# Kernel optimization log

Measured on AMD Instinct MI355X. Metric: run time of the kernel, lower is better.

## Reference

```python
import jax, jax.numpy as jnp
import numpy as np

EPS = 1e-8
N_ITER = 3
S = 8      # n_slots
D = 64     # slot_size
HID = 128  # mlp hidden


def _ln(x, w, b):
    m = jnp.mean(x, axis=-1, keepdims=True)
    v = jnp.var(x, axis=-1, keepdims=True)
    return (x - m) * jax.lax.rsqrt(v + 1e-5) * w + b


def setup_inputs() -> dict:
    key = jax.random.key(0)
    ks = jax.random.split(key, 20)
    B, N, Din = 128, 4096, 64
    g = lambda k, sh, s: (jax.random.normal(k, sh, jnp.float32) * s)
    return {
        "inputs": jax.random.normal(ks[0], (B, N, Din), jnp.float32),
        "eps_noise": jax.random.normal(ks[1], (B, S, D), jnp.float32),
        "slot_mu": g(ks[2], (1, 1, D), 0.1),
        "slot_logvar": g(ks[3], (1, 1, D), 0.1),
        "k_w": g(ks[4], (D, Din), 1.0 / np.sqrt(Din)),
        "v_w": g(ks[5], (D, Din), 1.0 / np.sqrt(Din)),
        "q_w": g(ks[6], (D, D), 1.0 / np.sqrt(D)),
        "ni_w": jnp.ones((Din,), jnp.float32), "ni_b": jnp.zeros((Din,), jnp.float32),
        "ns_w": jnp.ones((D,), jnp.float32),  "ns_b": jnp.zeros((D,), jnp.float32),
        "nr_w": jnp.ones((D,), jnp.float32),  "nr_b": jnp.zeros((D,), jnp.float32),
        "gru_wih": g(ks[7], (3 * D, D), 1.0 / np.sqrt(D)),
        "gru_whh": g(ks[8], (3 * D, D), 1.0 / np.sqrt(D)),
        "gru_bih": jnp.zeros((3 * D,), jnp.float32),
        "gru_bhh": jnp.zeros((3 * D,), jnp.float32),
        "mlp_w1": g(ks[9], (HID, D), 1.0 / np.sqrt(D)),
        "mlp_w2": g(ks[10], (D, HID), 1.0 / np.sqrt(HID)),
        "mlp_b2": jnp.zeros((D,), jnp.float32),
    }


def _gru(x, h, wih, whh, bih, bhh):
    gi = x @ wih.T + bih  # [BS, 3D]
    gh = h @ whh.T + bhh
    i_r, i_z, i_n = jnp.split(gi, 3, axis=-1)
    h_r, h_z, h_n = jnp.split(gh, 3, axis=-1)
    r = jax.nn.sigmoid(i_r + h_r)
    z = jax.nn.sigmoid(i_z + h_z)
    n = jnp.tanh(i_n + r * h_n)
    return (1.0 - z) * n + z * h


def _step(slots, k, v, q_w, ns_w, ns_b, nr_w, nr_b,
          gru_wih, gru_whh, gru_bih, gru_bhh, mlp_w1, mlp_w2, mlp_b2):
    B = slots.shape[0]
    q = _ln(slots, ns_w, ns_b) @ q_w.T                     # [B,S,D]
    logits = jnp.einsum('bnd,bsd->bns', k, q)              # [B,N,S]
    w = jax.nn.softmax(logits, axis=-1) + EPS              # softmax over slots
    w = w / jnp.sum(w, axis=-2, keepdims=True)             # renorm over tokens
    atten_maps = jnp.einsum('bns,bnd->bsd', w, v)          # [B,S,D]
    h = _gru(atten_maps.reshape(B * S, D), slots.reshape(B * S, D),
             gru_wih, gru_whh, gru_bih, gru_bhh)
    h = h + (jax.nn.relu(_ln(h, nr_w, nr_b) @ mlp_w1.T) @ mlp_w2.T + mlp_b2)
    return h.reshape(B, S, D), w


def reference(inputs, eps_noise, slot_mu, slot_logvar, k_w, v_w, q_w,
              ni_w, ni_b, ns_w, ns_b, nr_w, nr_b,
              gru_wih, gru_whh, gru_bih, gru_bhh, mlp_w1, mlp_w2, mlp_b2):
    std = jnp.exp(0.5 * slot_logvar)
    slots = slot_mu + std * eps_noise                      # [B,S,D]
    x = _ln(inputs, ni_w, ni_b)
    k = (x @ k_w.T) / np.sqrt(D).astype(np.float32)        # [B,N,D]
    v = x @ v_w.T
    args = (q_w, ns_w, ns_b, nr_w, nr_b, gru_wih, gru_whh,
            gru_bih, gru_bhh, mlp_w1, mlp_w2, mlp_b2)
    for _ in range(N_ITER):
        slots, w = _step(slots, k, v, *args)
    slots, w = _step(jax.lax.stop_gradient(slots), k, v, *args)
    return slots, w
```

## Files before the change

### kernel.cpp

```cpp
#include <hip/hip_runtime.h>
#include <hip/hip_bf16.h>

#define BB 128
#define NN 4096
#define DD 64
#define SS 8
#define HH 128

typedef __attribute__((ext_vector_type(8))) short short8;
typedef __attribute__((ext_vector_type(4))) float f32x4;

__device__ __forceinline__ float warp_red_sum(float v) {
    #pragma unroll
    for (int off = 32; off; off >>= 1) v += __shfl_xor(v, off);
    return v;
}

__device__ __forceinline__ float bcastlane(float v, int l) {
    return __int_as_float(__builtin_amdgcn_readlane(__float_as_int(v), l));
}

__device__ __forceinline__ unsigned short bfu(float f) {
    __hip_bfloat16 h = __float2bfloat16(f);
    return *(unsigned short*)&h;
}

__device__ __forceinline__ unsigned pk2(float a, float b) {
    return (unsigned)bfu(a) | ((unsigned)bfu(b) << 16);
}

__global__ __launch_bounds__(256) void prep_kernel(
    const float* __restrict__ v_w, const float* __restrict__ q_w,
    const float* __restrict__ wih, const float* __restrict__ whh,
    const float* __restrict__ w1, const float* __restrict__ w2,
    float* __restrict__ vwT, float* __restrict__ qwT,
    float* __restrict__ wihT, float* __restrict__ whhT,
    float* __restrict__ w1T, float* __restrict__ w2T)
{
    int i0 = blockIdx.x * blockDim.x + threadIdx.x;
    int nthr = gridDim.x * blockDim.x;
    for (int t = i0; t < 4096; t += nthr) {
        int i = t >> 6, o = t & 63;
        vwT[t] = v_w[o * 64 + i];
        qwT[t] = q_w[o * 64 + i];
    }
    for (int t = i0; t < 12288; t += nthr) {
        int r = t / 192, c = t % 192;
        wihT[t] = wih[c * 64 + r];
        whhT[t] = whh[c * 64 + r];
    }
    for (int t = i0; t < 8192; t += nthr) {
        int r = t >> 7, c = t & 127;
        w1T[t] = w1[c * 64 + r];
    }
    for (int t = i0; t < 8192; t += nthr) {
        int r = t >> 6, c = t & 63;
        w2T[t] = w2[c * 128 + r];
    }
}

__global__ __launch_bounds__(256) void init_q_kernel(
    const float* __restrict__ eps, const float* __restrict__ mu,
    const float* __restrict__ lv, const float* __restrict__ qwT,
    const float* __restrict__ k_w,
    const float* __restrict__ nsw, const float* __restrict__ nsb,
    float* __restrict__ slots, unsigned short* __restrict__ qb,
    float* __restrict__ zbuf)
{
    const int tid = threadIdx.x, lane = tid & 63;
    const int row = blockIdx.x * 4 + (tid >> 6);
    const int idx = row * 64 + lane;
    float s0 = mu[lane] + __expf(0.5f * lv[lane]) * eps[idx];
    slots[idx] = s0;
    float m = warp_red_sum(s0) * (1.0f / 64.0f);
    float dx = s0 - m;
    float var = warp_red_sum(dx * dx) * (1.0f / 64.0f);
    float xln = dx * rsqrtf(var + 1e-5f) * nsw[lane] + nsb[lane];
    float q = 0.f;
    #pragma unroll 8
    for (int i = 0; i < 64; ++i) q = fmaf(bcastlane(xln, i), qwT[i * 64 + lane], q);
    float qp = 0.f;
    #pragma unroll 8
    for (int o = 0; o < 64; ++o) qp = fmaf(bcastlane(q, o), k_w[o * 64 + lane], qp);
    qb[idx] = bfu(qp * 0.125f);
    int g = blockIdx.x * 256 + tid;
    for (int j = g; j < 66560; j += 65536) zbuf[j] = 0.f;
}

__global__ __launch_bounds__(256) void phase_a_ln(
    const float* __restrict__ inp, const float* __restrict__ niw, const float* __restrict__ nib,
    unsigned short* __restrict__ xb, unsigned short* __restrict__ xbt)
{
    __shared__ unsigned short xt[64 * 136];
    const int tid = threadIdx.x, lane = tid & 63, widx = tid >> 6;
    const int tg = lane >> 4, dq = lane & 15;
    const float4 wni = *(const float4*)&niw[dq * 4];
    const float4 bni = *(const float4*)&nib[dq * 4];
    const int tok0 = blockIdx.x * 128;
    #pragma unroll
    for (int it = 0; it < 8; ++it) {
        const int m = widx * 32 + it * 4 + tg;
        float4 x = *(const float4*)&inp[(size_t)(tok0 + m) * 64 + dq * 4];
        float s1 = x.x + x.y + x.z + x.w;
        float s2 = fmaf(x.x, x.x, fmaf(x.y, x.y, fmaf(x.z, x.z, x.w * x.w)));
        #pragma unroll
        for (int o = 1; o < 16; o <<= 1) { s1 += __shfl_xor(s1, o); s2 += __shfl_xor(s2, o); }
        float mean = s1 * (1.0f / 64.0f);
        float var = s2 * (1.0f / 64.0f) - mean * mean;
        float rstd = rsqrtf(var + 1e-5f);
        float y0 = (x.x - mean) * rstd * wni.x + bni.x;
        float y1 = (x.y - mean) * rstd * wni.y + bni.y;
        float y2 = (x.z - mean) * rstd * wni.z + bni.z;
        float y3 = (x.w - mean) * rstd * wni.w + bni.w;
        uint2 p; p.x = pk2(y0, y1); p.y = pk2(y2, y3);
        *(uint2*)&xb[(size_t)(tok0 + m) * 64 + dq * 4] = p;
        xt[(dq * 4 + 0) * 136 + m] = bfu(y0);
        xt[(dq * 4 + 1) * 136 + m] = bfu(y1);
        xt[(dq * 4 + 2) * 136 + m] = bfu(y2);
        xt[(dq * 4 + 3) * 136 + m] = bfu(y3);
    }
    __syncthreads();
    const int b = blockIdx.x >> 5, tin = (blockIdx.x & 31) * 128;
    const int d = tid >> 2, q4 = tid & 3;
    #pragma unroll
    for (int c = 0; c < 4; ++c) {
        uint4 o = *(uint4*)&xt[d * 136 + q4 * 32 + c * 8];
        *(uint4*)&xbt[((size_t)b * 64 + d) * 4096 + tin + q4 * 32 + c * 8] = o;
    }
}

__global__ __launch_bounds__(256) void attn_mfma(
    const __hip_bfloat16* __restrict__ xb, const unsigned short* __restrict__ xbt,
    const unsigned short* __restrict__ qb,
    float* __restrict__ numer, float* __restrict__ denom, float* __restrict__ wout)
{
    __shared__ unsigned short smem[24192];
    unsigned short* Qs = smem;
    const int tid = threadIdx.x, lane = tid & 63, widx = tid >> 6;
    unsigned short* wls = smem + 1152 + widx * 1152;
    unsigned short* vt  = smem + 5760 + widx * 4608;
    const int b = blockIdx.y;

    for (int t = tid; t < 1024; t += 256) {
        int s = t >> 6, dd = t & 63;
        Qs[s * 72 + dd] = (s < 8) ? qb[b * 512 + t] : (unsigned short)0;
    }
    for (int t = lane; t < 576; t += 64) wls[576 + t] = 0;
    __syncthreads();

    const int quad = lane >> 4, l16 = lane & 15;
    short8 bq0 = *(const short8*)&Qs[l16 * 72 + quad * 8];
    short8 bq1 = *(const short8*)&Qs[l16 * 72 + 32 + quad * 8];

    f32x4 accv[4];
    #pragma unroll
    for (int nt = 0; nt < 4; ++nt) accv[nt] = (f32x4){0.f, 0.f, 0.f, 0.f};
    float dsum = 0.f;

    const int twave0 = blockIdx.x * 512 + widx * 128;
    const int vd = lane >> 3, vc = (lane & 7) * 8;
    #pragma unroll
    for (int iter = 0; iter < 2; ++iter) {
        const int t0 = twave0 + iter * 64;
        uint4 vld[8];
        #pragma unroll
        for (int i = 0; i < 8; ++i)
            vld[i] = *(const uint4*)&xbt[((size_t)b * 64 + i * 8 + vd) * 4096 + t0 + vc];

        #pragma unroll
        for (int t4 = 0; t4 < 4; ++t4) {
            const size_t krow = ((size_t)b * NN + t0 + t4 * 16 + l16) * 64;
            short8 ak0 = *(const short8*)&xb[krow + quad * 8];
            short8 ak1 = *(const short8*)&xb[krow + 32 + quad * 8];
            f32x4 lg = (f32x4){0.f, 0.f, 0.f, 0.f};
            lg = __builtin_amdgcn_mfma_f32_16x16x32_bf16(ak0, bq0, lg, 0, 0, 0);
            lg = __builtin_amdgcn_mfma_f32_16x16x32_bf16(ak1, bq1, lg, 0, 0, 0);
            float wv[4];
            #pragma unroll
            for (int r = 0; r < 4; ++r) {
                float e = __expf(lg[r]);
                float s = e;
                s += __shfl_xor(s, 1); s += __shfl_xor(s, 2); s += __shfl_xor(s, 4);
                wv[r] = e / s + 1e-8f;
                dsum += wv[r];
            }
            if (l16 < 8) {
                *(unsigned*)&wls[l16 * 72 + t4 * 16 + quad * 4]     = pk2(wv[0], wv[1]);
                *(unsigned*)&wls[l16 * 72 + t4 * 16 + quad * 4 + 2] = pk2(wv[2], wv[3]);
                if (wout) {
                    float* wp = wout + ((size_t)b * NN + t0 + t4 * 16 + quad * 4) * 8 + l16;
                    wp[0] = wv[0]; wp[8] = wv[1]; wp[16] = wv[2]; wp[24] = wv[3];
                }
            }
        }
        #pragma unroll
        for (int i = 0; i < 8; ++i)
            *(uint4*)&vt[(i * 8 + vd) * 72 + vc] = vld[i];
        #pragma unroll
        for (int ks = 0; ks < 2; ++ks) {
            short8 aw = *(const short8*)&wls[l16 * 72 + ks * 32 + quad * 8];
            #pragma unroll
            for (int nt = 0; nt < 4; ++nt) {
                short8 bv = *(const short8*)&vt[(nt * 16 + l16) * 72 + ks * 32 + quad * 8];
                accv[nt] = __builtin_amdgcn_mfma_f32_16x16x32_bf16(aw, bv, accv[nt], 0, 0, 0);
            }
        }
    }
    dsum += __shfl_xor(dsum, 16);
    dsum += __shfl_xor(dsum, 32);
    __syncthreads();
    float* red = (float*)(smem + 5760);
    float* dred = red + 2048;
    if (quad < 2) {
        #pragma unroll
        for (int nt = 0; nt < 4; ++nt)
            #pragma unroll
            for (int r = 0; r < 4; ++r)
                red[widx * 512 + (quad * 4 + r) * 64 + nt * 16 + l16] = accv[nt][r];
    }
    if (quad == 0 && l16 < 8) dred[widx * 8 + l16] = dsum;
    __syncthreads();
    for (int e = tid; e < 512; e += 256)
        atomicAdd(numer + (size_t)b * 512 + e, red[e] + red[512 + e] + red[1024 + e] + red[1536 + e]);
    if (tid < 8)
        atomicAdd(denom + b * 8 + tid, dred[tid] + dred[8 + tid] + dred[16 + tid] + dred[24 + tid]);
}

__global__ __launch_bounds__(256) void gru_q_kernel(
    const float* __restrict__ numerX, const float* __restrict__ denom,
    const float* __restrict__ slotsIn,
    const float* __restrict__ vwT, const float* __restrict__ wihT, const float* __restrict__ whhT,
    const float* __restrict__ w1T, const float* __restrict__ w2T,
    const float* __restrict__ bih, const float* __restrict__ bhh,
    const float* __restrict__ nrw, const float* __restrict__ nrb,
    const float* __restrict__ b2,
    const float* __restrict__ qwT, const float* __restrict__ k_w,
    const float* __restrict__ nsw, const float* __restrict__ nsb,
    float* __restrict__ slotsOut, unsigned short* __restrict__ qb,
    float* __restrict__ zbuf)
{
    const int tid = threadIdx.x, lane = tid & 63;
    const int row = blockIdx.x * 4 + (tid >> 6);
    float nx = numerX[row * 64 + lane];
    float xp = 0.f;
    #pragma unroll 8
    for (int i = 0; i < 64; ++i) xp = fmaf(bcastlane(nx, i), vwT[i * 64 + lane], xp);
    float x = xp / denom[row];
    float h = slotsIn[row * 64 + lane];
    float air = 0, aiz = 0, ain = 0, ahr = 0, ahz = 0, ahn = 0;
    #pragma unroll 8
    for (int i = 0; i < 64; ++i) {
        float xi = bcastlane(x, i), hi = bcastlane(h, i);
        const float* wi = wihT + i * 192;
        const float* wh = whhT + i * 192;
        air = fmaf(xi, wi[lane], air);
        aiz = fmaf(xi, wi[64 + lane], aiz);
        ain = fmaf(xi, wi[128 + lane], ain);
        ahr = fmaf(hi, wh[lane], ahr);
        ahz = fmaf(hi, wh[64 + lane], ahz);
        ahn = fmaf(hi, wh[128 + lane], ahn);
    }
    air += bih[lane]; aiz += bih[64 + lane]; ain += bih[128 + lane];
    ahr += bhh[lane]; ahz += bhh[64 + lane]; ahn += bhh[128 + lane];
    float r = 1.f / (1.f + __expf(-(air + ahr)));
    float z = 1.f / (1.f + __expf(-(aiz + ahz)));
    float n = tanhf(ain + r * ahn);
    float hn = (1.f - z) * n + z * h;
    float m = warp_red_sum(hn) * (1.0f / 64.0f);
    float dx = hn - m;
    float var = warp_red_sum(dx * dx) * (1.0f / 64.0f);
    float u = dx * rsqrtf(var + 1e-5f) * nrw[lane] + nrb[lane];
    float o0 = 0.f, o1 = 0.f;
    #pragma unroll 8
    for (int i = 0; i < 64; ++i) {
        float ui = bcastlane(u, i);
        const float* w1r = w1T + i * 128;
        o0 = fmaf(ui, w1r[lane], o0);
        o1 = fmaf(ui, w1r[64 + lane], o1);
    }
    o0 = fmaxf(o0, 0.f); o1 = fmaxf(o1, 0.f);
    float y = 0.f;
    #pragma unroll 8
    for (int j = 0; j < 64; ++j) y = fmaf(bcastlane(o0, j), w2T[j * 64 + lane], y);
    #pragma unroll 8
    for (int j = 0; j < 64; ++j) y = fmaf(bcastlane(o1, j), w2T[(64 + j) * 64 + lane], y);
    y += b2[lane];
    float out = hn + y;
    slotsOut[row * 64 + lane] = out;
    float m2 = warp_red_sum(out) * (1.0f / 64.0f);
    float dx2 = out - m2;
    float var2 = warp_red_sum(dx2 * dx2) * (1.0f / 64.0f);
    float u2 = dx2 * rsqrtf(var2 + 1e-5f) * nsw[lane] + nsb[lane];
    float q = 0.f;
    #pragma unroll 8
    for (int i = 0; i < 64; ++i) q = fmaf(bcastlane(u2, i), qwT[i * 64 + lane], q);
    float qp = 0.f;
    #pragma unroll 8
    for (int o = 0; o < 64; ++o) qp = fmaf(bcastlane(q, o), k_w[o * 64 + lane], qp);
    qb[row * 64 + lane] = bfu(qp * 0.125f);
    int g = blockIdx.x * 256 + tid;
    for (int j = g; j < 66560; j += 65536) zbuf[j] = 0.f;
}

__global__ __launch_bounds__(256) void renorm_kernel(float* __restrict__ wout,
                                                     const float* __restrict__ denom)
{
    const size_t i4 = (size_t)blockIdx.x * blockDim.x + threadIdx.x;
    const size_t b = i4 >> 13;
    const int half = (int)(i4 & 1);
    float4 v = reinterpret_cast<float4*>(wout)[i4];
    const float4 dv = reinterpret_cast<const float4*>(denom)[b * 2 + half];
    v.x /= dv.x; v.y /= dv.y; v.z /= dv.z; v.w /= dv.w;
    reinterpret_cast<float4*>(wout)[i4] = v;
}

extern "C" void kernel_launch(void* const* d_in, const int* in_sizes, int n_in,
                              void* d_out, int out_size, void* d_ws, size_t ws_size,
                              hipStream_t stream)
{
    const float* inputs  = (const float*)d_in[0];
    const float* eps_n   = (const float*)d_in[1];
    const float* mu      = (const float*)d_in[2];
    const float* lv      = (const float*)d_in[3];
    const float* k_w     = (const float*)d_in[4];
    const float* v_w     = (const float*)d_in[5];
    const float* q_w     = (const float*)d_in[6];
    const float* ni_w    = (const float*)d_in[7];
    const float* ni_b    = (const float*)d_in[8];
    const float* ns_w    = (const float*)d_in[9];
    const float* ns_b    = (const float*)d_in[10];
    const float* nr_w    = (const float*)d_in[11];
    const float* nr_b    = (const float*)d_in[12];
    const float* gru_wih = (const float*)d_in[13];
    const float* gru_whh = (const float*)d_in[14];
    const float* gru_bih = (const float*)d_in[15];
    const float* gru_bhh = (const float*)d_in[16];
    const float* mlp_w1  = (const float*)d_in[17];
    const float* mlp_w2  = (const float*)d_in[18];
    const float* mlp_b2  = (const float*)d_in[19];

    char* wsb = (char*)d_ws;
    unsigned short* xb  = (unsigned short*)wsb;
    unsigned short* xbt = (unsigned short*)(wsb + 67108864);
    float* f      = (float*)(wsb + 134217728);
    float* slotsA = f;
    float* slotsB = f + 65536;
    unsigned short* qb = (unsigned short*)(f + 131072);
    float* numer0 = f + 163840;
    float* denom0 = f + 229376;
    float* numer1 = f + 230400;
    float* denom1 = f + 295936;
    float* vwT    = f + 296960;
    float* qwT    = f + 301056;
    float* wihT   = f + 305152;
    float* whhT   = f + 317440;
    float* w1T    = f + 329728;
    float* w2T    = f + 337920;

    float* out_slots = (float*)d_out;
    float* out_w     = out_slots + 65536;

    prep_kernel<<<64, 256, 0, stream>>>(v_w, q_w, gru_wih, gru_whh, mlp_w1, mlp_w2,
                                        vwT, qwT, wihT, whhT, w1T, w2T);
    init_q_kernel<<<256, 256, 0, stream>>>(eps_n, mu, lv, qwT, k_w, ns_w, ns_b,
                                           slotsA, qb, numer0);
    phase_a_ln<<<4096, 256, 0, stream>>>(inputs, ni_w, ni_b, xb, xbt);

    float* cur = slotsA;
    float* numers[2] = {numer0, numer1};
    float* denoms[2] = {denom0, denom1};
    for (int step = 0; step < 4; ++step) {
        int pb = step & 1;
        attn_mfma<<<dim3(8, 128), 256, 0, stream>>>((const __hip_bfloat16*)xb, xbt, qb,
                                                    numers[pb], denoms[pb],
                                                    step == 3 ? out_w : nullptr);
        float* nxt = (step == 3) ? out_slots : ((step & 1) ? slotsA : slotsB);
        gru_q_kernel<<<256, 256, 0, stream>>>(numers[pb], denoms[pb], cur,
                                              vwT, wihT, whhT, w1T, w2T,
                                              gru_bih, gru_bhh, nr_w, nr_b, mlp_b2,
                                              qwT, k_w, ns_w, ns_b,
                                              nxt, qb, numers[1 - pb]);
        cur = nxt;
    }
    renorm_kernel<<<4096, 256, 0, stream>>>(out_w, denom1);
}
```

Baseline: 456.1 us.

## Swap MFMA operands so slots map to rows, and swizzle LN transpose LDS

The logits MFMA now takes Q as the A operand and K as B, so each lane holds four slot values for one token. The softmax over slots then needs one cross-lane shuffle instead of three per element, uses a reciprocal instead of a divide, and writes the weight output as a float4 per token. The LayerNorm transpose buffer gets an XOR swizzle to cut LDS bank conflicts on the scattered column writes. Denominator sums are reduced per slot across 16 lanes at the end, and the wls store pattern changes to scattered 16-bit writes.

```diff
diff --git a/kernel.cpp b/kernel.cpp
--- a/kernel.cpp
+++ b/kernel.cpp
@@ -97,6 +97,7 @@
     const float4 wni = *(const float4*)&niw[dq * 4];
     const float4 bni = *(const float4*)&nib[dq * 4];
     const int tok0 = blockIdx.x * 128;
+    const int sw = dq & 7;
     #pragma unroll
     for (int it = 0; it < 8; ++it) {
         const int m = widx * 32 + it * 4 + tg;
@@ -114,18 +115,21 @@
         float y3 = (x.w - mean) * rstd * wni.w + bni.w;
         uint2 p; p.x = pk2(y0, y1); p.y = pk2(y2, y3);
         *(uint2*)&xb[(size_t)(tok0 + m) * 64 + dq * 4] = p;
-        xt[(dq * 4 + 0) * 136 + m] = bfu(y0);
-        xt[(dq * 4 + 1) * 136 + m] = bfu(y1);
-        xt[(dq * 4 + 2) * 136 + m] = bfu(y2);
-        xt[(dq * 4 + 3) * 136 + m] = bfu(y3);
+        const int col = ((((m >> 3) ^ sw) << 3) | (m & 7));
+        xt[(dq * 4 + 0) * 136 + col] = bfu(y0);
+        xt[(dq * 4 + 1) * 136 + col] = bfu(y1);
+        xt[(dq * 4 + 2) * 136 + col] = bfu(y2);
+        xt[(dq * 4 + 3) * 136 + col] = bfu(y3);
     }
     __syncthreads();
     const int b = blockIdx.x >> 5, tin = (blockIdx.x & 31) * 128;
     const int d = tid >> 2, q4 = tid & 3;
+    const int sr = (d >> 2) & 7;
     #pragma unroll
     for (int c = 0; c < 4; ++c) {
-        uint4 o = *(uint4*)&xt[d * 136 + q4 * 32 + c * 8];
-        *(uint4*)&xbt[((size_t)b * 64 + d) * 4096 + tin + q4 * 32 + c * 8] = o;
+        const int cc = q4 * 4 + c;
+        uint4 o = *(uint4*)&xt[d * 136 + ((cc ^ sr) << 3)];
+        *(uint4*)&xbt[((size_t)b * 64 + d) * 4096 + tin + cc * 8] = o;
     }
 }
 
@@ -149,13 +153,13 @@
     __syncthreads();
 
     const int quad = lane >> 4, l16 = lane & 15;
-    short8 bq0 = *(const short8*)&Qs[l16 * 72 + quad * 8];
-    short8 bq1 = *(const short8*)&Qs[l16 * 72 + 32 + quad * 8];
+    short8 aq0 = *(const short8*)&Qs[l16 * 72 + quad * 8];
+    short8 aq1 = *(const short8*)&Qs[l16 * 72 + 32 + quad * 8];
 
     f32x4 accv[4];
     #pragma unroll
     for (int nt = 0; nt < 4; ++nt) accv[nt] = (f32x4){0.f, 0.f, 0.f, 0.f};
-    float dsum = 0.f;
+    float dacc[4] = {0.f, 0.f, 0.f, 0.f};
 
     const int twave0 = blockIdx.x * 512 + widx * 128;
     const int vd = lane >> 3, vc = (lane & 7) * 8;
@@ -169,28 +173,29 @@
 
         #pragma unroll
         for (int t4 = 0; t4 < 4; ++t4) {
-            const size_t krow = ((size_t)b * NN + t0 + t4 * 16 + l16) * 64;
-            short8 ak0 = *(const short8*)&xb[krow + quad * 8];
-            short8 ak1 = *(const short8*)&xb[krow + 32 + quad * 8];
+            const int tok = t0 + t4 * 16 + l16;
+            const size_t xrow = ((size_t)b * NN + tok) * 64;
+            short8 bk0 = *(const short8*)&xb[xrow + quad * 8];
+            short8 bk1 = *(const short8*)&xb[xrow + 32 + quad * 8];
             f32x4 lg = (f32x4){0.f, 0.f, 0.f, 0.f};
-            lg = __builtin_amdgcn_mfma_f32_16x16x32_bf16(ak0, bq0, lg, 0, 0, 0);
-            lg = __builtin_amdgcn_mfma_f32_16x16x32_bf16(ak1, bq1, lg, 0, 0, 0);
+            lg = __builtin_amdgcn_mfma_f32_16x16x32_bf16(aq0, bk0, lg, 0, 0, 0);
+            lg = __builtin_amdgcn_mfma_f32_16x16x32_bf16(aq1, bk1, lg, 0, 0, 0);
+            float e[4];
+            #pragma unroll
+            for (int r = 0; r < 4; ++r) e[r] = __expf(lg[r]);
+            float s4 = (e[0] + e[1]) + (e[2] + e[3]);
+            float stot = s4 + __shfl_xor(s4, 16);
+            float rs = __builtin_amdgcn_rcpf(stot);
             float wv[4];
             #pragma unroll
-            for (int r = 0; r < 4; ++r) {
-                float e = __expf(lg[r]);
-                float s = e;
-                s += __shfl_xor(s, 1); s += __shfl_xor(s, 2); s += __shfl_xor(s, 4);
-                wv[r] = e / s + 1e-8f;
-                dsum += wv[r];
-            }
-            if (l16 < 8) {
-                *(unsigned*)&wls[l16 * 72 + t4 * 16 + quad * 4]     = pk2(wv[0], wv[1]);
-                *(unsigned*)&wls[l16 * 72 + t4 * 16 + quad * 4 + 2] = pk2(wv[2], wv[3]);
-                if (wout) {
-                    float* wp = wout + ((size_t)b * NN + t0 + t4 * 16 + quad * 4) * 8 + l16;
-                    wp[0] = wv[0]; wp[8] = wv[1]; wp[16] = wv[2]; wp[24] = wv[3];
-                }
+            for (int r = 0; r < 4; ++r) { wv[r] = fmaf(e[r], rs, 1e-8f); dacc[r] += wv[r]; }
+            if (quad < 2) {
+                #pragma unroll
+                for (int r = 0; r < 4; ++r)
+                    wls[(quad * 4 + r) * 72 + t4 * 16 + l16] = bfu(wv[r]);
+                if (wout)
+                    *(float4*)&wout[((size_t)b * NN + tok) * 8 + quad * 4] =
+                        make_float4(wv[0], wv[1], wv[2], wv[3]);
             }
         }
         #pragma unroll
@@ -206,8 +211,13 @@
             }
         }
     }
-    dsum += __shfl_xor(dsum, 16);
-    dsum += __shfl_xor(dsum, 32);
+    #pragma unroll
+    for (int r = 0; r < 4; ++r) {
+        dacc[r] += __shfl_xor(dacc[r], 1);
+        dacc[r] += __shfl_xor(dacc[r], 2);
+        dacc[r] += __shfl_xor(dacc[r], 4);
+        dacc[r] += __shfl_xor(dacc[r], 8);
+    }
     __syncthreads();
     float* red = (float*)(smem + 5760);
     float* dred = red + 2048;
@@ -217,8 +227,11 @@
             #pragma unroll
             for (int r = 0; r < 4; ++r)
                 red[widx * 512 + (quad * 4 + r) * 64 + nt * 16 + l16] = accv[nt][r];
-    }
-    if (quad == 0 && l16 < 8) dred[widx * 8 + l16] = dsum;
+        if (l16 == 0) {
+            #pragma unroll
+            for (int r = 0; r < 4; ++r) dred[widx * 8 + quad * 4 + r] = dacc[r];
+        }
+    }
     __syncthreads();
     for (int e = tid; e < 512; e += 256)
         atomicAdd(numer + (size_t)b * 512 + e, red[e] + red[512 + e] + red[1024 + e] + red[1536 + e]);
```

After: 448.1 us. No clear change (-1.7%).
